# Kernel optimization log

Measured on AMD Instinct MI355X. Metric: run time of the kernel, lower is better.

Reference implementation:

```python
import jax, jax.numpy as jnp
import numpy as np
from jax import lax

B, EMB, HEADS, HD, LAYERS, FIX, ADAPT, MLP, NCLS = 32, 768, 12, 64, 12, 6, 6, 3072, 100
PE_N, PE_D = 100, 256
SCALE = 1.0 / np.sqrt(HD)


def _ln(x, g, b, eps=1e-5):
    m = jnp.mean(x, axis=-1, keepdims=True)
    v = jnp.mean((x - m) ** 2, axis=-1, keepdims=True)
    return (x - m) / jnp.sqrt(v + eps) * g + b


def _vit_block(x, g1, b1, qkvw, qkvb, pw, pb, g2, b2, f1w, f1b, f2w, f2b):
    Bn, N, _ = x.shape
    h = _ln(x, g1, b1)
    qkv = (h @ qkvw + qkvb).reshape(Bn, N, 3, HEADS, HD)
    q, k, v = [qkv[:, :, i].transpose(0, 2, 1, 3) for i in range(3)]  # [B,H,N,hd]
    attn = jax.nn.softmax(jnp.einsum('bhqd,bhkd->bhqk', q, k) * SCALE, axis=-1)
    o = jnp.einsum('bhqk,bhkd->bhqd', attn, v).transpose(0, 2, 1, 3).reshape(Bn, N, EMB)
    x = x + (o @ pw + pb)
    h = _ln(x, g2, b2)
    return x + (jax.nn.gelu(h @ f1w + f1b, approximate=False) @ f2w + f2b)


def _sinusoid_table():
    pos = np.arange(PE_N)[:, None].astype(np.float64)
    j = np.arange(PE_D)[None, :]
    ang = pos / np.power(10000.0, 2 * (j // 2) / PE_D)
    tab = ang.copy()
    tab[:, 0::2] = np.sin(ang[:, 0::2])
    tab[:, 1::2] = np.cos(ang[:, 1::2])
    return jnp.asarray(tab, dtype=jnp.float32)


def setup_inputs() -> dict:
    key = jax.random.key(0)
    ks = iter(jax.random.split(key, 40))
    r = lambda shape: jax.random.normal(next(ks), shape, dtype=jnp.float32) * 0.02
    inp = {
        'x': jax.random.normal(next(ks), (B, 3, 224, 224), dtype=jnp.float32),
        'budget': jax.random.uniform(next(ks), (B,), dtype=jnp.float32),
        'pe_table': _sinusoid_table(),
        'lat_w1': r((PE_D, EMB)), 'lat_b1': r((EMB,)),
        'lat_ln_g': jnp.ones((EMB,), jnp.float32), 'lat_ln_b': jnp.zeros((EMB,), jnp.float32),
        'lat_w2': r((EMB, EMB)), 'lat_b2': r((EMB,)),
        'patch_w': r((EMB, 3, 16, 16)), 'patch_b': r((EMB,)),
        'cls_token': r((1, 1, EMB)), 'pos_embed': r((1, 198, EMB)),
        'sched_w': r((EMB, ADAPT)), 'sched_b': r((ADAPT,)),
        'ln1_g': jnp.ones((LAYERS, EMB), jnp.float32), 'ln1_b': jnp.zeros((LAYERS, EMB), jnp.float32),
        'qkv_w': r((LAYERS, EMB, 3 * EMB)), 'qkv_b': r((LAYERS, 3 * EMB)),
        'proj_w': r((LAYERS, EMB, EMB)), 'proj_b': r((LAYERS, EMB)),
        'ln2_g': jnp.ones((LAYERS, EMB), jnp.float32), 'ln2_b': jnp.zeros((LAYERS, EMB), jnp.float32),
        'fc1_w': r((LAYERS, EMB, MLP)), 'fc1_b': r((LAYERS, MLP)),
        'fc2_w': r((LAYERS, MLP, EMB)), 'fc2_b': r((LAYERS, EMB)),
        'norm_g': jnp.ones((EMB,), jnp.float32), 'norm_b': jnp.zeros((EMB,), jnp.float32),
        'head_w': r((EMB, NCLS)), 'head_b': r((NCLS,)),
    }
    return inp


def reference(x, budget, pe_table, lat_w1, lat_b1, lat_ln_g, lat_ln_b, lat_w2, lat_b2,
              patch_w, patch_b, cls_token, pos_embed, sched_w, sched_b,
              ln1_g, ln1_b, qkv_w, qkv_b, proj_w, proj_b, ln2_g, ln2_b,
              fc1_w, fc1_b, fc2_w, fc2_b, norm_g, norm_b, head_w, head_b):
    Bn = x.shape[0]
    bud = lax.stop_gradient(budget)
    # latency encoder
    idx = jnp.round(bud * (PE_N - 1)).astype(jnp.int32)
    h = pe_table[idx] @ lat_w1 + lat_b1
    h = jax.nn.gelu(h, approximate=False)
    h = _ln(h, lat_ln_g, lat_ln_b)
    lat = (h @ lat_w2 + lat_b2)[:, None, :]  # [B,1,EMB]
    # patch embed: conv16 s16 -> [B,EMB,14,14]
    p = lax.conv_general_dilated(x, patch_w, (16, 16), 'VALID',
                                 dimension_numbers=('NCHW', 'OIHW', 'NCHW'))
    p = (p + patch_b[None, :, None, None]).reshape(Bn, EMB, 196).transpose(0, 2, 1)
    tok = jnp.concatenate([lat, jnp.broadcast_to(cls_token, (Bn, 1, EMB)), p], axis=1)
    tok = tok + pos_embed  # [B,198,EMB]
    blk = lambda t, i: _vit_block(t, ln1_g[i], ln1_b[i], qkv_w[i], qkv_b[i], proj_w[i], proj_b[i],
                                  ln2_g[i], ln2_b[i], fc1_w[i], fc1_b[i], fc2_w[i], fc2_b[i])
    for i in range(FIX):
        tok = blk(tok, i)
    # layer routing (eval path): per-sample top-k over adaptive layers
    logits = tok[:, 0] @ sched_w + sched_b  # [B,ADAPT]
    k = jnp.maximum(jnp.ceil(bud * ADAPT).astype(jnp.int32), 1)  # [B]
    ranks = jnp.argsort(jnp.argsort(-logits, axis=-1), axis=-1)
    active = ranks < k[:, None]  # [B,ADAPT] bool
    t = tok[:, 1:]  # drop latency token -> [B,197,EMB]
    for i in range(ADAPT):
        out = blk(t, FIX + i)
        t = jnp.where(active[:, i, None, None], out, t)
    t = _ln(t, norm_g, norm_b)
    return t[:, 0] @ head_w + head_b
```

## Files before the change

kernel.cpp:

```cpp
#include <hip/hip_runtime.h>
#include <hip/hip_bf16.h>
#include <math.h>


using bf16   = __hip_bfloat16;
using short8 = __attribute__((ext_vector_type(8))) short;
using f32x4  = __attribute__((ext_vector_type(4))) float;

#define GLD16(gptr, lptr)                                                            \
    __builtin_amdgcn_global_load_lds((const __attribute__((address_space(1))) void*)(gptr), \
                                     (__attribute__((address_space(3))) void*)(lptr), 16, 0, 0)

__device__ __forceinline__ void split2(float x, short& h, short& l)
{
    unsigned u  = __float_as_uint(x);
    unsigned hr = (u + 0x7fffu + ((u >> 16) & 1u)) & 0xffff0000u;
    h = (short)(hr >> 16);
    float res = x - __uint_as_float(hr);
    l = (short)(__float_as_uint(res) >> 16);
}

__global__ __launch_bounds__(256) void trans_split_kernel(const float* __restrict__ W,
                                                          short* __restrict__ Wh,
                                                          short* __restrict__ Wl,
                                                          int K, int N)
{
    __shared__ float tile[32][33];
    int n0 = blockIdx.x * 32, k0 = blockIdx.y * 32;
    int c = threadIdx.x & 31, r = threadIdx.x >> 5;
    #pragma unroll
    for (int i = 0; i < 32; i += 8)
        tile[r + i][c] = W[(size_t)(k0 + r + i) * N + n0 + c];
    __syncthreads();
    #pragma unroll
    for (int i = 0; i < 32; i += 8) {
        short h, l; split2(tile[c][r + i], h, l);
        size_t o = (size_t)(n0 + r + i) * K + k0 + c;
        Wh[o] = h; Wl[o] = l;
    }
}

__global__ void split_kernel(const float* __restrict__ in, short* __restrict__ h,
                             short* __restrict__ l, int n)
{
    int i = blockIdx.x * 256 + threadIdx.x;
    if (i >= n) return;
    short hh, ll; split2(in[i], hh, ll);
    h[i] = hh; l[i] = ll;
}

__global__ void im2col_split_kernel(const float* __restrict__ x,
                                    short* __restrict__ Ah, short* __restrict__ Al)
{
    int idx = blockIdx.x * 256 + threadIdx.x;
    if (idx >= 6272 * 768) return;
    int k = idx % 768;
    int row = idx / 768;
    int b = row / 196, p = row % 196;
    int py = p / 14, px = p % 14;
    int c = k >> 8, rem = k & 255;
    int i = rem >> 4, j = rem & 15;
    float v = x[(((size_t)b * 3 + c) * 224 + py * 16 + i) * 224 + px * 16 + j];
    short h, l; split2(v, h, l);
    Ah[idx] = h; Al[idx] = l;
}

template<int BN, bool GELU, bool RES, bool SPLITOUT>
__global__ __launch_bounds__(256) void gemm3_kernel(const short* __restrict__ Ah,
                                                    const short* __restrict__ Al,
                                                    const short* __restrict__ Bh,
                                                    const short* __restrict__ Bl,
                                                    const float* __restrict__ bias,
                                                    const float* __restrict__ resid,
                                                    float* __restrict__ Cf,
                                                    short* __restrict__ Ch,
                                                    short* __restrict__ Cl,
                                                    int M, int N, int K)
{
    constexpr int AL_OFF = 4096;
    constexpr int BH_OFF = 8192;
    constexpr int BL_OFF = 8192 + BN * 32;
    constexpr int BUFSZ  = 8192 + BN * 64;
    constexpr int MI     = (BN == 128) ? 4 : 2;
    __shared__ __align__(16) short sm[2 * BUFSZ];
    const int tid  = threadIdx.x;
    const int lane = tid & 63;
    const int w    = tid >> 6;
    const int wm   = (BN == 128) ? (w >> 1) : w;
    const int wn   = (BN == 128) ? (w & 1) : 0;

    const int gx  = gridDim.x;
    const int nwg = gx * gridDim.y;
    const int wg  = blockIdx.y * gx + blockIdx.x;
    const int qq  = nwg >> 3, rr = nwg & 7;
    const int xcd = wg & 7, seq = wg >> 3;
    const int work = (xcd < rr ? xcd * (qq + 1) : rr * (qq + 1) + (xcd - rr) * qq) + seq;
    const int m0   = (work / gx) * 128;
    const int n0   = (work % gx) * BN;

    const int col  = lane & 15;
    const int quad = lane >> 4;
    const int srow = lane >> 2;
    const int skc  = (((lane & 3) ^ ((lane >> 3) & 3)) * 8);
    const int rswz = (quad ^ ((col >> 1) & 3)) * 8;

    f32x4 acc[MI][4];
    #pragma unroll
    for (int i = 0; i < MI; ++i)
        #pragma unroll
        for (int j = 0; j < 4; ++j) acc[i][j] = (f32x4)0.f;

    const short* Ahb = Ah + (size_t)m0 * K;
    const short* Alb = Al + (size_t)m0 * K;
    const short* Bhb = Bh + (size_t)n0 * K;
    const short* Blb = Bl + (size_t)n0 * K;

    auto stage = [&](int buf, int t) {
        const int k0 = t << 5;
        short* dst = &sm[buf * BUFSZ];
        #pragma unroll
        for (int i = 0; i < 2; ++i) {
            int r = w * 32 + i * 16;
            size_t go = (size_t)(r + srow) * K + k0 + skc;
            GLD16(Ahb + go, dst + r * 32);
            GLD16(Alb + go, dst + AL_OFF + r * 32);
            if (BN == 128) {
                GLD16(Bhb + go, dst + BH_OFF + r * 32);
                GLD16(Blb + go, dst + BL_OFF + r * 32);
            }
        }
        if (BN == 64) {
            int r = w * 16;
            size_t go = (size_t)(r + srow) * K + k0 + skc;
            GLD16(Bhb + go, dst + BH_OFF + r * 32);
            GLD16(Blb + go, dst + BL_OFF + r * 32);
        }
    };

    auto compute = [&](int buf) {
        const short* cb = &sm[buf * BUFSZ];
        short8 ah[MI], al[MI];
        #pragma unroll
        for (int mi = 0; mi < MI; ++mi) {
            int ao = (wm * (MI * 16) + mi * 16 + col) * 32 + rswz;
            ah[mi] = *(const short8*)(cb + ao);
            al[mi] = *(const short8*)(cb + AL_OFF + ao);
        }
        #pragma unroll
        for (int ni = 0; ni < 4; ++ni) {
            int bo = ((BN == 128 ? wn * 64 : 0) + ni * 16 + col) * 32 + rswz;
            short8 bh = *(const short8*)(cb + BH_OFF + bo);
            short8 bl = *(const short8*)(cb + BL_OFF + bo);
            #pragma unroll
            for (int mi = 0; mi < MI; ++mi) {
                acc[mi][ni] = __builtin_amdgcn_mfma_f32_16x16x32_bf16(ah[mi], bh, acc[mi][ni], 0, 0, 0);
                acc[mi][ni] = __builtin_amdgcn_mfma_f32_16x16x32_bf16(al[mi], bh, acc[mi][ni], 0, 0, 0);
                acc[mi][ni] = __builtin_amdgcn_mfma_f32_16x16x32_bf16(ah[mi], bl, acc[mi][ni], 0, 0, 0);
            }
        }
    };

    const int nk = K >> 5;
    stage(0, 0);
    __syncthreads();
    int cur = 0;
    for (int t = 0; t < nk - 1; ++t) {
        stage(cur ^ 1, t + 1);
        compute(cur);
        __syncthreads();
        cur ^= 1;
    }
    compute(cur);

    #pragma unroll
    for (int mi = 0; mi < MI; ++mi) {
        #pragma unroll
        for (int ni = 0; ni < 4; ++ni) {
            int gcol = n0 + (BN == 128 ? wn * 64 : 0) + ni * 16 + col;
            float bv = bias[gcol];
            #pragma unroll
            for (int r = 0; r < 4; ++r) {
                int grow = m0 + wm * (MI * 16) + mi * 16 + quad * 4 + r;
                if (grow < M) {
                    float v = acc[mi][ni][r] + bv;
                    if (RES) v += resid[(size_t)grow * N + gcol];
                    if (GELU) v = 0.5f * v * (1.f + erff(v * 0.70710678118654752f));
                    size_t o = (size_t)grow * N + gcol;
                    if (SPLITOUT) { short h, l; split2(v, h, l); Ch[o] = h; Cl[o] = l; }
                    else          Cf[o] = v;
                }
            }
        }
    }
}

__global__ __launch_bounds__(256) void ln_kernel(const float* __restrict__ x,
                                                 const float* __restrict__ g,
                                                 const float* __restrict__ bta,
                                                 short* __restrict__ outh,
                                                 short* __restrict__ outl, int M)
{
    int row = blockIdx.x * 4 + (threadIdx.x >> 6);
    int lane = threadIdx.x & 63;
    if (row >= M) return;
    const float* xr = x + (size_t)row * 768;
    float vals[12];
    float s = 0.f;
    #pragma unroll
    for (int i = 0; i < 12; ++i) { vals[i] = xr[lane + i * 64]; s += vals[i]; }
    #pragma unroll
    for (int off = 32; off; off >>= 1) s += __shfl_xor(s, off);
    float mean = s * (1.f / 768.f);
    float vs = 0.f;
    #pragma unroll
    for (int i = 0; i < 12; ++i) { float d = vals[i] - mean; vs += d * d; }
    #pragma unroll
    for (int off = 32; off; off >>= 1) vs += __shfl_xor(vs, off);
    float rstd = rsqrtf(vs * (1.f / 768.f) + 1e-5f);
    size_t rb = (size_t)row * 768;
    #pragma unroll
    for (int i = 0; i < 12; ++i) {
        int c = lane + i * 64;
        short h, l; split2((vals[i] - mean) * rstd * g[c] + bta[c], h, l);
        outh[rb + c] = h; outl[rb + c] = l;
    }
}

__global__ __launch_bounds__(128) void attn_kernel(const float* __restrict__ qkv,
                                                   short* __restrict__ Oh,
                                                   short* __restrict__ Ol, int S)
{
    __shared__ float Ks[64 * 64];
    __shared__ float Vs[64 * 64];
    int blk  = blockIdx.x;
    int bh   = blk >> 1, half = blk & 1;
    int b = bh / 12, h = bh % 12;
    int halfRows = (S + 1) >> 1;
    int q0   = half * halfRows;
    int qcnt = min(halfRows, S - q0);
    const float* base = qkv + (size_t)b * S * 2304;
    int tid = threadIdx.x;
    int r = q0 + tid;
    bool act = (tid < qcnt);
    float q[64];
    #pragma unroll
    for (int d = 0; d < 64; ++d) q[d] = 0.f;
    if (act) {
        const float4* qp = (const float4*)(base + (size_t)r * 2304 + h * 64);
        #pragma unroll
        for (int d4 = 0; d4 < 16; ++d4) {
            float4 t = qp[d4];
            q[4 * d4] = t.x; q[4 * d4 + 1] = t.y; q[4 * d4 + 2] = t.z; q[4 * d4 + 3] = t.w;
        }
    }
    float o[64];
    #pragma unroll
    for (int d = 0; d < 64; ++d) o[d] = 0.f;
    float m = -1e30f, l = 0.f;

    for (int jc = 0; jc < S; jc += 64) {
        int cnt = min(64, S - jc);
        __syncthreads();
        for (int idx = tid; idx < cnt * 16; idx += 128) {
            int j = idx >> 4, d4 = idx & 15;
            const float4* rp = (const float4*)(base + (size_t)(jc + j) * 2304 + h * 64) + d4;
            ((float4*)Ks)[j * 16 + d4] = rp[192];
            ((float4*)Vs)[j * 16 + d4] = rp[384];
        }
        __syncthreads();
        if (act) {
            for (int j0 = 0; j0 < cnt; j0 += 8) {
                float sc[8];
                float pm = -1e30f;
                #pragma unroll
                for (int jj = 0; jj < 8; ++jj) {
                    int j = j0 + jj;
                    const float4* kr = (const float4*)&Ks[j * 64];
                    float s0 = 0.f, s1 = 0.f, s2 = 0.f, s3 = 0.f;
                    #pragma unroll
                    for (int d4 = 0; d4 < 16; ++d4) {
                        float4 kv = kr[d4];
                        s0 += q[4 * d4]     * kv.x;
                        s1 += q[4 * d4 + 1] * kv.y;
                        s2 += q[4 * d4 + 2] * kv.z;
                        s3 += q[4 * d4 + 3] * kv.w;
                    }
                    float sv = ((s0 + s1) + (s2 + s3)) * 0.125f;
                    sv = (j < cnt) ? sv : -1e30f;
                    sc[jj] = sv;
                    pm = fmaxf(pm, sv);
                }
                if (!__all(pm <= m + 8.f)) {
                    float mn = fmaxf(m, pm);
                    float alpha = __expf(m - mn);
                    l *= alpha;
                    #pragma unroll
                    for (int d = 0; d < 64; ++d) o[d] *= alpha;
                    m = mn;
                }
                #pragma unroll
                for (int jj = 0; jj < 8; ++jj) {
                    float p = __expf(sc[jj] - m);
                    l += p;
                    const float4* vr = (const float4*)&Vs[(j0 + jj) * 64];
                    #pragma unroll
                    for (int d4 = 0; d4 < 16; ++d4) {
                        float4 vv = vr[d4];
                        o[4 * d4]     += p * vv.x;
                        o[4 * d4 + 1] += p * vv.y;
                        o[4 * d4 + 2] += p * vv.z;
                        o[4 * d4 + 3] += p * vv.w;
                    }
                }
            }
        }
    }
    if (act) {
        float inv = 1.f / l;
        size_t rb = (size_t)(b * S + r) * 768 + h * 64;
        #pragma unroll
        for (int d = 0; d < 64; ++d) {
            short hh, ll; split2(o[d] * inv, hh, ll);
            Oh[rb + d] = hh; Ol[rb + d] = ll;
        }
    }
}

__global__ __launch_bounds__(256) void latent1_kernel(const float* __restrict__ pe_table,
                                                      const float* __restrict__ budget,
                                                      const float* __restrict__ w1,
                                                      const float* __restrict__ b1,
                                                      float* __restrict__ hout)
{
    int b = blockIdx.x, tid = threadIdx.x;
    __shared__ float pe[256];
    int idx = (int)rintf(budget[b] * 99.f);
    pe[tid] = pe_table[idx * 256 + tid];
    __syncthreads();
    int col = blockIdx.y * 256 + tid;
    float a = b1[col];
    for (int k = 0; k < 256; ++k) a += pe[k] * w1[k * 768 + col];
    hout[b * 768 + col] = 0.5f * a * (1.f + erff(a * 0.70710678118654752f));
}

__global__ __launch_bounds__(256) void ln32_kernel(const float* __restrict__ x,
                                                   const float* __restrict__ g,
                                                   const float* __restrict__ bta,
                                                   float* __restrict__ outp)
{
    int row = blockIdx.x * 4 + (threadIdx.x >> 6);
    int lane = threadIdx.x & 63;
    const float* xr = x + (size_t)row * 768;
    float vals[12];
    float s = 0.f;
    #pragma unroll
    for (int i = 0; i < 12; ++i) { vals[i] = xr[lane + i * 64]; s += vals[i]; }
    #pragma unroll
    for (int off = 32; off; off >>= 1) s += __shfl_xor(s, off);
    float mean = s * (1.f / 768.f);
    float vs = 0.f;
    #pragma unroll
    for (int i = 0; i < 12; ++i) { float d = vals[i] - mean; vs += d * d; }
    #pragma unroll
    for (int off = 32; off; off >>= 1) vs += __shfl_xor(vs, off);
    float rstd = rsqrtf(vs * (1.f / 768.f) + 1e-5f);
    size_t rb = (size_t)row * 768;
    #pragma unroll
    for (int i = 0; i < 12; ++i) {
        int c = lane + i * 64;
        outp[rb + c] = (vals[i] - mean) * rstd * g[c] + bta[c];
    }
}

__global__ __launch_bounds__(256) void latent2_kernel(const float* __restrict__ hn,
                                                      const float* __restrict__ w2,
                                                      const float* __restrict__ b2,
                                                      float* __restrict__ lat)
{
    int b = blockIdx.x, tid = threadIdx.x;
    __shared__ float hrow[768];
    for (int i = tid; i < 768; i += 256) hrow[i] = hn[b * 768 + i];
    __syncthreads();
    int col = blockIdx.y * 256 + tid;
    float a = b2[col];
    for (int k = 0; k < 768; ++k) a += hrow[k] * w2[k * 768 + col];
    lat[b * 768 + col] = a;
}

__global__ void assemble_kernel(const float* __restrict__ lat, const float* __restrict__ cls,
                                const float* __restrict__ P, const float* __restrict__ pos,
                                float* __restrict__ T)
{
    int idx = blockIdx.x * 256 + threadIdx.x;
    if (idx >= 32 * 198 * 768) return;
    int c = idx % 768;
    int row = idx / 768;
    int b = row / 198, t = row % 198;
    float v;
    if (t == 0)      v = lat[b * 768 + c];
    else if (t == 1) v = cls[c];
    else             v = P[((size_t)b * 196 + (t - 2)) * 768 + c];
    T[idx] = v + pos[t * 768 + c];
}

__global__ void sched_kernel(const float* __restrict__ T, const float* __restrict__ sw,
                             const float* __restrict__ sb, const float* __restrict__ budget,
                             int* __restrict__ active)
{
    int b = blockIdx.x, lane = threadIdx.x;
    const float* xr = T + (size_t)b * 198 * 768;
    float acc[6] = {0, 0, 0, 0, 0, 0};
    for (int k = lane; k < 768; k += 64) {
        float xv = xr[k];
        #pragma unroll
        for (int i = 0; i < 6; ++i) acc[i] += xv * sw[k * 6 + i];
    }
    #pragma unroll
    for (int i = 0; i < 6; ++i)
        #pragma unroll
        for (int off = 32; off; off >>= 1) acc[i] += __shfl_xor(acc[i], off);
    if (lane == 0) {
        float lg[6];
        #pragma unroll
        for (int i = 0; i < 6; ++i) lg[i] = acc[i] + sb[i];
        int k = (int)ceilf(budget[b] * 6.f);
        if (k < 1) k = 1;
        for (int i = 0; i < 6; ++i) {
            int rank = 0;
            for (int j = 0; j < 6; ++j)
                rank += (lg[j] > lg[i]) || (lg[j] == lg[i] && j < i);
            active[b * 6 + i] = (rank < k) ? 1 : 0;
        }
    }
}

__global__ void droplat_kernel(const float* __restrict__ T, float* __restrict__ T2)
{
    int idx = blockIdx.x * 256 + threadIdx.x;
    if (idx >= 32 * 197 * 768) return;
    int c = idx % 768;
    int row = idx / 768;
    int b = row / 197, t = row % 197;
    T2[idx] = T[((size_t)b * 198 + t + 1) * 768 + c];
}

__global__ void select_kernel(float* __restrict__ T2, const float* __restrict__ OUT,
                              const int* __restrict__ active, int layer)
{
    int idx = blockIdx.x * 256 + threadIdx.x;
    if (idx >= 32 * 197 * 768) return;
    int b = idx / (197 * 768);
    if (active[b * 6 + layer]) T2[idx] = OUT[idx];
}

__global__ __launch_bounds__(128) void head_kernel(const float* __restrict__ T2,
                                                   const float* __restrict__ g,
                                                   const float* __restrict__ bta,
                                                   const float* __restrict__ hw,
                                                   const float* __restrict__ hb,
                                                   float* __restrict__ out)
{
    int b = blockIdx.x, tid = threadIdx.x;
    __shared__ float hn[768];
    __shared__ float red[128];
    const float* xr = T2 + (size_t)b * 197 * 768;
    float v[6];
    float s = 0.f;
    #pragma unroll
    for (int i = 0; i < 6; ++i) { v[i] = xr[tid + i * 128]; s += v[i]; }
    red[tid] = s; __syncthreads();
    for (int o = 64; o > 0; o >>= 1) { if (tid < o) red[tid] += red[tid + o]; __syncthreads(); }
    float mean = red[0] * (1.f / 768.f);
    __syncthreads();
    float vs = 0.f;
    #pragma unroll
    for (int i = 0; i < 6; ++i) { float d = v[i] - mean; vs += d * d; }
    red[tid] = vs; __syncthreads();
    for (int o = 64; o > 0; o >>= 1) { if (tid < o) red[tid] += red[tid + o]; __syncthreads(); }
    float rstd = rsqrtf(red[0] * (1.f / 768.f) + 1e-5f);
    #pragma unroll
    for (int i = 0; i < 6; ++i) {
        int c = tid + i * 128;
        hn[c] = (v[i] - mean) * rstd * g[c] + bta[c];
    }
    __syncthreads();
    if (tid < 100) {
        float a = hb[tid];
        for (int k = 0; k < 768; ++k) a += hn[k] * hw[k * 100 + tid];
        out[b * 100 + tid] = a;
    }
}

extern "C" void kernel_launch(void* const* d_in, const int* in_sizes, int n_in,
                              void* d_out, int out_size, void* d_ws, size_t ws_size,
                              hipStream_t stream)
{
    const float* x        = (const float*)d_in[0];
    const float* budget   = (const float*)d_in[1];
    const float* pe_table = (const float*)d_in[2];
    const float* lat_w1   = (const float*)d_in[3];
    const float* lat_b1   = (const float*)d_in[4];
    const float* lat_ln_g = (const float*)d_in[5];
    const float* lat_ln_b = (const float*)d_in[6];
    const float* lat_w2   = (const float*)d_in[7];
    const float* lat_b2   = (const float*)d_in[8];
    const float* patch_w  = (const float*)d_in[9];
    const float* patch_b  = (const float*)d_in[10];
    const float* cls_tok  = (const float*)d_in[11];
    const float* pos_emb  = (const float*)d_in[12];
    const float* sched_w  = (const float*)d_in[13];
    const float* sched_b  = (const float*)d_in[14];
    const float* ln1_g    = (const float*)d_in[15];
    const float* ln1_b    = (const float*)d_in[16];
    const float* qkv_w    = (const float*)d_in[17];
    const float* qkv_b    = (const float*)d_in[18];
    const float* proj_w   = (const float*)d_in[19];
    const float* proj_b   = (const float*)d_in[20];
    const float* ln2_g    = (const float*)d_in[21];
    const float* ln2_b    = (const float*)d_in[22];
    const float* fc1_w    = (const float*)d_in[23];
    const float* fc1_b    = (const float*)d_in[24];
    const float* fc2_w    = (const float*)d_in[25];
    const float* fc2_b    = (const float*)d_in[26];
    const float* norm_g   = (const float*)d_in[27];
    const float* norm_b   = (const float*)d_in[28];
    const float* head_w   = (const float*)d_in[29];
    const float* head_b   = (const float*)d_in[30];
    float* out = (float*)d_out;
    (void)in_sizes; (void)n_in; (void)out_size; (void)ws_size;

    char* ws = (char*)d_ws;
    size_t off = 0;
    auto alloc = [&](size_t bytes) -> char* {
        char* p = ws + off;
        off = (off + bytes + 255) & ~(size_t)255;
        return p;
    };
    short* sQKVh = (short*)alloc(2304ull * 768 * 2);
    short* sQKVl = (short*)alloc(2304ull * 768 * 2);
    short* sPRJh = (short*)alloc(768ull * 768 * 2);
    short* sPRJl = (short*)alloc(768ull * 768 * 2);
    short* sFC1h = (short*)alloc(3072ull * 768 * 2);
    short* sFC1l = (short*)alloc(3072ull * 768 * 2);
    short* sFC2h = (short*)alloc(768ull * 3072 * 2);
    short* sFC2l = (short*)alloc(768ull * 3072 * 2);
    short* pwh   = (short*)alloc(768ull * 768 * 2);
    short* pwl   = (short*)alloc(768ull * 768 * 2);
    float* T     = (float*)alloc(6400ull * 768 * 4);
    float* T2    = (float*)alloc(6400ull * 768 * 4);
    float* OUT   = (float*)alloc(6400ull * 768 * 4);
    short* Hh    = (short*)alloc(6400ull * 768 * 2);
    short* Hl    = (short*)alloc(6400ull * 768 * 2);
    float* QKV   = (float*)alloc(6336ull * 2304 * 4);
    short* Oh    = (short*)alloc(6400ull * 768 * 2);
    short* Ol    = (short*)alloc(6400ull * 768 * 2);
    short* Mh    = (short*)alloc(6400ull * 3072 * 2);
    short* Ml    = (short*)alloc(6400ull * 3072 * 2);
    float* lat   = (float*)alloc(32ull * 768 * 4);
    float* latH  = (float*)alloc(32ull * 768 * 4);
    float* latN  = (float*)alloc(32ull * 768 * 4);
    int*   act   = (int*)alloc(32 * 6 * 4);
    float* P     = QKV;
    short* Aph   = Mh;
    short* Apl   = Ml;

    im2col_split_kernel<<<(6272 * 768 + 255) / 256, 256, 0, stream>>>(x, Aph, Apl);
    split_kernel<<<(768 * 768 + 255) / 256, 256, 0, stream>>>(patch_w, pwh, pwl, 768 * 768);
    latent1_kernel<<<dim3(32, 3), 256, 0, stream>>>(pe_table, budget, lat_w1, lat_b1, latH);
    ln32_kernel<<<8, 256, 0, stream>>>(latH, lat_ln_g, lat_ln_b, latN);
    latent2_kernel<<<dim3(32, 3), 256, 0, stream>>>(latN, lat_w2, lat_b2, lat);
    gemm3_kernel<64, false, false, false><<<dim3(12, 49), 256, 0, stream>>>(
        Aph, Apl, pwh, pwl, patch_b, nullptr, P, nullptr, nullptr, 6272, 768, 768);
    assemble_kernel<<<(32 * 198 * 768 + 255) / 256, 256, 0, stream>>>(lat, cls_tok, P, pos_emb, T);

    for (int l = 0; l < 6; ++l) {
        trans_split_kernel<<<dim3(72, 24), 256, 0, stream>>>(qkv_w + (size_t)l * 768 * 2304, sQKVh, sQKVl, 768, 2304);
        trans_split_kernel<<<dim3(24, 24), 256, 0, stream>>>(proj_w + (size_t)l * 768 * 768, sPRJh, sPRJl, 768, 768);
        trans_split_kernel<<<dim3(96, 24), 256, 0, stream>>>(fc1_w + (size_t)l * 768 * 3072, sFC1h, sFC1l, 768, 3072);
        trans_split_kernel<<<dim3(24, 96), 256, 0, stream>>>(fc2_w + (size_t)l * 3072 * 768, sFC2h, sFC2l, 3072, 768);

        ln_kernel<<<6336 / 4, 256, 0, stream>>>(T, ln1_g + l * 768, ln1_b + l * 768, Hh, Hl, 6336);
        gemm3_kernel<128, false, false, false><<<dim3(18, 50), 256, 0, stream>>>(
            Hh, Hl, sQKVh, sQKVl, qkv_b + l * 2304, nullptr, QKV, nullptr, nullptr, 6336, 2304, 768);
        attn_kernel<<<768, 128, 0, stream>>>(QKV, Oh, Ol, 198);
        gemm3_kernel<64, false, true, false><<<dim3(12, 50), 256, 0, stream>>>(
            Oh, Ol, sPRJh, sPRJl, proj_b + l * 768, T, T, nullptr, nullptr, 6336, 768, 768);
        ln_kernel<<<6336 / 4, 256, 0, stream>>>(T, ln2_g + l * 768, ln2_b + l * 768, Hh, Hl, 6336);
        gemm3_kernel<128, true, false, true><<<dim3(24, 50), 256, 0, stream>>>(
            Hh, Hl, sFC1h, sFC1l, fc1_b + l * 3072, nullptr, nullptr, Mh, Ml, 6336, 3072, 768);
        gemm3_kernel<64, false, true, false><<<dim3(12, 50), 256, 0, stream>>>(
            Mh, Ml, sFC2h, sFC2l, fc2_b + l * 768, T, T, nullptr, nullptr, 6336, 768, 3072);
    }

    sched_kernel<<<32, 64, 0, stream>>>(T, sched_w, sched_b, budget, act);
    droplat_kernel<<<(32 * 197 * 768 + 255) / 256, 256, 0, stream>>>(T, T2);

    for (int i = 0; i < 6; ++i) {
        int l = 6 + i;
        trans_split_kernel<<<dim3(72, 24), 256, 0, stream>>>(qkv_w + (size_t)l * 768 * 2304, sQKVh, sQKVl, 768, 2304);
        trans_split_kernel<<<dim3(24, 24), 256, 0, stream>>>(proj_w + (size_t)l * 768 * 768, sPRJh, sPRJl, 768, 768);
        trans_split_kernel<<<dim3(96, 24), 256, 0, stream>>>(fc1_w + (size_t)l * 768 * 3072, sFC1h, sFC1l, 768, 3072);
        trans_split_kernel<<<dim3(24, 96), 256, 0, stream>>>(fc2_w + (size_t)l * 3072 * 768, sFC2h, sFC2l, 3072, 768);

        ln_kernel<<<6304 / 4, 256, 0, stream>>>(T2, ln1_g + l * 768, ln1_b + l * 768, Hh, Hl, 6304);
        gemm3_kernel<128, false, false, false><<<dim3(18, 50), 256, 0, stream>>>(
            Hh, Hl, sQKVh, sQKVl, qkv_b + l * 2304, nullptr, QKV, nullptr, nullptr, 6304, 2304, 768);
        attn_kernel<<<768, 128, 0, stream>>>(QKV, Oh, Ol, 197);
        gemm3_kernel<64, false, true, false><<<dim3(12, 50), 256, 0, stream>>>(
            Oh, Ol, sPRJh, sPRJl, proj_b + l * 768, T2, OUT, nullptr, nullptr, 6304, 768, 768);
        ln_kernel<<<6304 / 4, 256, 0, stream>>>(OUT, ln2_g + l * 768, ln2_b + l * 768, Hh, Hl, 6304);
        gemm3_kernel<128, true, false, true><<<dim3(24, 50), 256, 0, stream>>>(
            Hh, Hl, sFC1h, sFC1l, fc1_b + l * 3072, nullptr, nullptr, Mh, Ml, 6304, 3072, 768);
        gemm3_kernel<64, false, true, false><<<dim3(12, 50), 256, 0, stream>>>(
            Mh, Ml, sFC2h, sFC2l, fc2_b + l * 768, OUT, OUT, nullptr, nullptr, 6304, 768, 3072);
        select_kernel<<<(32 * 197 * 768 + 255) / 256, 256, 0, stream>>>(T2, OUT, act, i);
    }

    head_kernel<<<32, 128, 0, stream>>>(T2, norm_g, norm_b, head_w, head_b, out);
}
```

Before: 7.029 ms.

## Split attention over key halves with merge kernel; triple-buffer BN=64 GEMM

```diff
diff --git a/kernel.cpp b/kernel.cpp
--- a/kernel.cpp
+++ b/kernel.cpp
@@ -10,6 +10,14 @@
 #define GLD16(gptr, lptr)                                                            \
     __builtin_amdgcn_global_load_lds((const __attribute__((address_space(1))) void*)(gptr), \
                                      (__attribute__((address_space(3))) void*)(lptr), 16, 0, 0)
+
+#define WAIT_BARRIER(N)                                          \
+    do {                                                         \
+        asm volatile("s_waitcnt vmcnt(" #N ")" ::: "memory");    \
+        __builtin_amdgcn_sched_barrier(0);                       \
+        __builtin_amdgcn_s_barrier();                            \
+        __builtin_amdgcn_sched_barrier(0);                       \
+    } while (0)
 
 __device__ __forceinline__ void split2(float x, short& h, short& l)
 {
@@ -81,8 +89,9 @@
     constexpr int BH_OFF = 8192;
     constexpr int BL_OFF = 8192 + BN * 32;
     constexpr int BUFSZ  = 8192 + BN * 64;
+    constexpr int NBUF   = (BN == 64) ? 3 : 2;
     constexpr int MI     = (BN == 128) ? 4 : 2;
-    __shared__ __align__(16) short sm[2 * BUFSZ];
+    __shared__ __align__(16) short sm[NBUF * BUFSZ];
     const int tid  = threadIdx.x;
     const int lane = tid & 63;
     const int w    = tid >> 6;
@@ -115,9 +124,8 @@
     const short* Bhb = Bh + (size_t)n0 * K;
     const short* Blb = Bl + (size_t)n0 * K;
 
-    auto stage = [&](int buf, int t) {
+    auto stage = [&](short* dst, int t) {
         const int k0 = t << 5;
-        short* dst = &sm[buf * BUFSZ];
         #pragma unroll
         for (int i = 0; i < 2; ++i) {
             int r = w * 32 + i * 16;
@@ -137,8 +145,7 @@
         }
     };
 
-    auto compute = [&](int buf) {
-        const short* cb = &sm[buf * BUFSZ];
+    auto compute = [&](const short* cb) {
         short8 ah[MI], al[MI];
         #pragma unroll
         for (int mi = 0; mi < MI; ++mi) {
@@ -161,16 +168,32 @@
     };
 
     const int nk = K >> 5;
-    stage(0, 0);
-    __syncthreads();
-    int cur = 0;
-    for (int t = 0; t < nk - 1; ++t) {
-        stage(cur ^ 1, t + 1);
-        compute(cur);
+    if constexpr (BN == 64) {
+        short *p0 = sm, *p1 = sm + BUFSZ, *p2 = sm + 2 * BUFSZ;
+        stage(p0, 0);
+        stage(p1, 1);
+        WAIT_BARRIER(6);
+        for (int t = 0; t + 2 < nk; ++t) {
+            stage(p2, t + 2);
+            compute(p0);
+            WAIT_BARRIER(6);
+            short* tmp = p0; p0 = p1; p1 = p2; p2 = tmp;
+        }
+        compute(p0);
+        WAIT_BARRIER(0);
+        compute(p1);
+    } else {
+        stage(sm, 0);
         __syncthreads();
-        cur ^= 1;
-    }
-    compute(cur);
+        int cur = 0;
+        for (int t = 0; t < nk - 1; ++t) {
+            stage(&sm[(cur ^ 1) * BUFSZ], t + 1);
+            compute(&sm[cur * BUFSZ]);
+            __syncthreads();
+            cur ^= 1;
+        }
+        compute(&sm[cur * BUFSZ]);
+    }
 
     #pragma unroll
     for (int mi = 0; mi < MI; ++mi) {
@@ -226,18 +249,22 @@
     }
 }
 
-__global__ __launch_bounds__(128) void attn_kernel(const float* __restrict__ qkv,
-                                                   short* __restrict__ Oh,
-                                                   short* __restrict__ Ol, int S)
+__global__ __launch_bounds__(128) void attn_part_kernel(const float* __restrict__ qkv,
+                                                        float* __restrict__ Op,
+                                                        float* __restrict__ Mp,
+                                                        float* __restrict__ Lp, int S)
 {
     __shared__ float Ks[64 * 64];
     __shared__ float Vs[64 * 64];
-    int blk  = blockIdx.x;
-    int bh   = blk >> 1, half = blk & 1;
+    int blk   = blockIdx.x;
+    int khalf = blk & 1, qhalf = (blk >> 1) & 1;
+    int bh = blk >> 2;
     int b = bh / 12, h = bh % 12;
-    int halfRows = (S + 1) >> 1;
-    int q0   = half * halfRows;
-    int qcnt = min(halfRows, S - q0);
+    int halfS = (S + 1) >> 1;
+    int q0   = qhalf * halfS;
+    int qcnt = min(halfS, S - q0);
+    int k0   = khalf * halfS;
+    int kcnt = min(halfS, S - k0);
     const float* base = qkv + (size_t)b * S * 2304;
     int tid = threadIdx.x;
     int r = q0 + tid;
@@ -258,12 +285,12 @@
     for (int d = 0; d < 64; ++d) o[d] = 0.f;
     float m = -1e30f, l = 0.f;
 
-    for (int jc = 0; jc < S; jc += 64) {
-        int cnt = min(64, S - jc);
+    for (int jc = 0; jc < kcnt; jc += 64) {
+        int cnt = min(64, kcnt - jc);
         __syncthreads();
         for (int idx = tid; idx < cnt * 16; idx += 128) {
             int j = idx >> 4, d4 = idx & 15;
-            const float4* rp = (const float4*)(base + (size_t)(jc + j) * 2304 + h * 64) + d4;
+            const float4* rp = (const float4*)(base + (size_t)(k0 + jc + j) * 2304 + h * 64) + d4;
             ((float4*)Ks)[j * 16 + d4] = rp[192];
             ((float4*)Vs)[j * 16 + d4] = rp[384];
         }
@@ -316,14 +343,34 @@
         }
     }
     if (act) {
-        float inv = 1.f / l;
-        size_t rb = (size_t)(b * S + r) * 768 + h * 64;
-        #pragma unroll
-        for (int d = 0; d < 64; ++d) {
-            short hh, ll; split2(o[d] * inv, hh, ll);
-            Oh[rb + d] = hh; Ol[rb + d] = ll;
-        }
-    }
+        size_t prow = (size_t)(khalf * 6400 + b * S + r);
+        float* op = Op + prow * 768 + h * 64;
+        #pragma unroll
+        for (int d = 0; d < 64; ++d) op[d] = o[d];
+        Mp[prow * 12 + h] = m;
+        Lp[prow * 12 + h] = l;
+    }
+}
+
+__global__ void attn_merge_kernel(const float* __restrict__ Op,
+                                  const float* __restrict__ Mp,
+                                  const float* __restrict__ Lp,
+                                  short* __restrict__ Oh, short* __restrict__ Ol,
+                                  int M)
+{
+    int idx = blockIdx.x * 256 + threadIdx.x;
+    if (idx >= M * 768) return;
+    int row = idx / 768;
+    int h   = (idx % 768) >> 6;
+    float m1 = Mp[(size_t)row * 12 + h],          m2 = Mp[(size_t)(6400 + row) * 12 + h];
+    float l1 = Lp[(size_t)row * 12 + h],          l2 = Lp[(size_t)(6400 + row) * 12 + h];
+    float mm = fmaxf(m1, m2);
+    float a1 = __expf(m1 - mm), a2 = __expf(m2 - mm);
+    float inv = 1.f / (l1 * a1 + l2 * a2);
+    float v = (Op[(size_t)row * 768 + (idx % 768)] * a1 +
+               Op[(size_t)(6400 + row) * 768 + (idx % 768)] * a2) * inv;
+    short hh, ll; split2(v, hh, ll);
+    Oh[idx] = hh; Ol[idx] = ll;
 }
 
 __global__ __launch_bounds__(256) void latent1_kernel(const float* __restrict__ pe_table,
@@ -563,6 +610,9 @@
     float* P     = QKV;
     short* Aph   = Mh;
     short* Apl   = Ml;
+    float* Opart = (float*)Mh;
+    float* Mpart = (float*)Ml;
+    float* Lpart = Mpart + 2 * 6400 * 12;
 
     im2col_split_kernel<<<(6272 * 768 + 255) / 256, 256, 0, stream>>>(x, Aph, Apl);
     split_kernel<<<(768 * 768 + 255) / 256, 256, 0, stream>>>(patch_w, pwh, pwl, 768 * 768);
@@ -582,7 +632,8 @@
         ln_kernel<<<6336 / 4, 256, 0, stream>>>(T, ln1_g + l * 768, ln1_b + l * 768, Hh, Hl, 6336);
         gemm3_kernel<128, false, false, false><<<dim3(18, 50), 256, 0, stream>>>(
             Hh, Hl, sQKVh, sQKVl, qkv_b + l * 2304, nullptr, QKV, nullptr, nullptr, 6336, 2304, 768);
-        attn_kernel<<<768, 128, 0, stream>>>(QKV, Oh, Ol, 198);
+        attn_part_kernel<<<1536, 128, 0, stream>>>(QKV, Opart, Mpart, Lpart, 198);
+        attn_merge_kernel<<<(6336 * 768 + 255) / 256, 256, 0, stream>>>(Opart, Mpart, Lpart, Oh, Ol, 6336);
         gemm3_kernel<64, false, true, false><<<dim3(12, 50), 256, 0, stream>>>(
             Oh, Ol, sPRJh, sPRJl, proj_b + l * 768, T, T, nullptr, nullptr, 6336, 768, 768);
         ln_kernel<<<6336 / 4, 256, 0, stream>>>(T, ln2_g + l * 768, ln2_b + l * 768, Hh, Hl, 6336);
@@ -605,7 +656,8 @@
         ln_kernel<<<6304 / 4, 256, 0, stream>>>(T2, ln1_g + l * 768, ln1_b + l * 768, Hh, Hl, 6304);
         gemm3_kernel<128, false, false, false><<<dim3(18, 50), 256, 0, stream>>>(
             Hh, Hl, sQKVh, sQKVl, qkv_b + l * 2304, nullptr, QKV, nullptr, nullptr, 6304, 2304, 768);
-        attn_kernel<<<768, 128, 0, stream>>>(QKV, Oh, Ol, 197);
+        attn_part_kernel<<<1536, 128, 0, stream>>>(QKV, Opart, Mpart, Lpart, 197);
+        attn_merge_kernel<<<(6304 * 768 + 255) / 256, 256, 0, stream>>>(Opart, Mpart, Lpart, Oh, Ol, 6304);
         gemm3_kernel<64, false, true, false><<<dim3(12, 50), 256, 0, stream>>>(
             Oh, Ol, sPRJh, sPRJl, proj_b + l * 768, T2, OUT, nullptr, nullptr, 6304, 768, 768);
         ln_kernel<<<6304 / 4, 256, 0, stream>>>(OUT, ln2_g + l * 768, ln2_b + l * 768, Hh, Hl, 6304);
```

Result: slower. 7.859 ms (+11.8%).
